# Kernel tuning notes

Hardware: AMD Instinct MI355X
Metric: run time of the kernel (lower is better)

## Reference

```python
import jax, jax.numpy as jnp
import numpy as np

N_NODES = 50000
N_EDGES = 800000
IN_DIM = 128
HGC = 128
LG = 3
K = 3
N_CLASSES = 10
BN_EPS = 1e-5


def setup_inputs() -> dict:
    key = jax.random.key(0)
    ks = jax.random.split(key, 16)
    inp = {
        "features": jax.random.normal(ks[0], (N_NODES, IN_DIM), dtype=jnp.float32),
        "edge_index": jax.random.randint(ks[1], (2, N_EDGES), 0, N_NODES, dtype=jnp.int64),
        "edge_weight": jax.random.uniform(ks[2], (N_EDGES,), dtype=jnp.float32),
    }
    # ChebConv weights: one (K, in, out) stack per layer (PyG: K separate bias-free Linears)
    dims = [IN_DIM] + [HGC] * LG
    for i in range(LG):
        fan_in = dims[i]
        inp[f"W{i}"] = jax.random.normal(ks[3 + i], (K, dims[i], dims[i + 1]), dtype=jnp.float32) * np.sqrt(2.0 / fan_in)
    # classifier head: Linear(HGC,256) -> ReLU -> BatchNorm1d(256) -> Linear(256, num_classes)
    inp["Wc1"] = jax.random.normal(ks[8], (HGC, 256), dtype=jnp.float32) * np.sqrt(2.0 / HGC)
    inp["bc1"] = jnp.zeros((256,), dtype=jnp.float32)
    inp["gamma"] = jnp.ones((256,), dtype=jnp.float32)
    inp["beta"] = jnp.zeros((256,), dtype=jnp.float32)
    inp["Wc2"] = jax.random.normal(ks[9], (256, N_CLASSES), dtype=jnp.float32) * np.sqrt(2.0 / 256)
    inp["bc2"] = jnp.zeros((N_CLASSES,), dtype=jnp.float32)
    return inp


def _scaled_laplacian_weights(edge_index, edge_weight, n_nodes):
    # get_laplacian(sym): L = I - D^{-1/2} A D^{-1/2}; ChebConv scales 2L/lambda_max - I
    # with lambda_max = 2.0 -> L_hat off-diagonal weights = -A_norm, diagonal = 0.
    row, col = edge_index[0], edge_index[1]
    deg = jax.ops.segment_sum(edge_weight, row, num_segments=n_nodes)
    dinv = jnp.where(deg > 0, jax.lax.rsqrt(jnp.maximum(deg, 1e-30)), 0.0)
    return -dinv[row] * edge_weight * dinv[col]


def _propagate(x, row, col, w, n_nodes):
    # SpMM: (L_hat @ x)[i] = sum_e w[e] * x[col[e]] for row[e]==i
    return jax.ops.segment_sum(w[:, None] * x[col], row, num_segments=n_nodes)


def _cheb_conv(x, W, row, col, w, n_nodes):
    # W: (K, in, out). Chebyshev recursion T0=x, T1=Lx, Tk=2LT_{k-1}-T_{k-2}
    Tx0 = x
    out = Tx0 @ W[0]
    Tx1 = _propagate(Tx0, row, col, w, n_nodes)
    out = out + Tx1 @ W[1]
    for k in range(2, W.shape[0]):
        Tx2 = 2.0 * _propagate(Tx1, row, col, w, n_nodes) - Tx0
        out = out + Tx2 @ W[k]
        Tx0, Tx1 = Tx1, Tx2
    return out


def reference(features, edge_index, edge_weight, W0, W1, W2, Wc1, bc1, gamma, beta, Wc2, bc2):
    n = features.shape[0]
    row, col = edge_index[0], edge_index[1]
    w = _scaled_laplacian_weights(edge_index, edge_weight, n)
    x = features
    for W in (W0, W1, W2):
        x = jax.nn.relu(_cheb_conv(x, W, row, col, w, n))  # dropout is identity in eval
    h = jax.nn.relu(x @ Wc1 + bc1)
    mean = jnp.mean(h, axis=0)
    var = jnp.var(h, axis=0)  # biased, as torch BatchNorm1d normalization
    h = (h - mean) * jax.lax.rsqrt(var + BN_EPS) * gamma + beta
    logit = h @ Wc2 + bc2
    return (logit, edge_weight)
```

## Files before the change

kernel.cpp:

```cpp
#include <hip/hip_runtime.h>
#include <cstdint>
#include <cstddef>

#define DIM 128
#define BN_EPS 1e-5f
#define NS 8

typedef short bf16x8 __attribute__((ext_vector_type(8)));
typedef float f32x4 __attribute__((ext_vector_type(4)));

__device__ __forceinline__ unsigned short f2bf(float f) {
  unsigned u = __float_as_uint(f);
  u = (u + 0x7fffu + ((u >> 16) & 1u)) >> 16;
  return (unsigned short)u;
}
__device__ __forceinline__ float bf2f(unsigned v) {
  return __uint_as_float(v << 16);
}


__global__ void deg_hist_kernel(const int* __restrict__ ei, const float* __restrict__ ew,
                                float* __restrict__ degS, int* __restrict__ countS, int E,
                                int N) {
  int e = blockIdx.x * blockDim.x + threadIdx.x;
  int g = blockIdx.x & (NS - 1);
  if (e < E) {
    int r = ei[e];
    atomicAdd(&degS[(size_t)g * N + r], ew[e]);
    atomicAdd(&countS[(size_t)g * N + r], 1);
  }
}

__global__ void reduce_dinv_kernel(const float* __restrict__ degS, float* __restrict__ dinv,
                                   int N) {
  int i = blockIdx.x * blockDim.x + threadIdx.x;
  if (i < N) {
    float d = 0.f;
#pragma unroll
    for (int g = 0; g < NS; ++g) d += degS[(size_t)g * N + i];
    dinv[i] = d > 0.f ? rsqrtf(fmaxf(d, 1e-30f)) : 0.f;
  }
}

__global__ __launch_bounds__(512) void scan_a_kernel(const int* __restrict__ countS,
                                                     int* __restrict__ off2,
                                                     int* __restrict__ bsums, int n8, int N) {
  __shared__ int sd[512];
  int t = threadIdx.x;
  int i = blockIdx.x * 512 + t;
  int v = 0;
  if (i < n8) {
    int g = i & (NS - 1), r = i >> 3;
    v = countS[(size_t)g * N + r];
  }
  sd[t] = v;
  __syncthreads();
  for (int off = 1; off < 512; off <<= 1) {
    int x = (t >= off) ? sd[t - off] : 0;
    __syncthreads();
    sd[t] += x;
    __syncthreads();
  }
  if (i < n8) off2[i] = sd[t] - v;
  if (t == 511) bsums[blockIdx.x] = sd[511];
}

__global__ __launch_bounds__(1024) void scan_b_kernel(int* __restrict__ bsums, int nb) {
  __shared__ int sd[1024];
  int t = threadIdx.x;
  int v = (t < nb) ? bsums[t] : 0;
  sd[t] = v;
  __syncthreads();
  for (int off = 1; off < 1024; off <<= 1) {
    int x = (t >= off) ? sd[t - off] : 0;
    __syncthreads();
    sd[t] += x;
    __syncthreads();
  }
  if (t < nb) bsums[t] = sd[t] - v;
}

__global__ __launch_bounds__(512) void scan_c_kernel(int* __restrict__ off2,
                                                     const int* __restrict__ bsums, int n8) {
  int i = blockIdx.x * 512 + threadIdx.x;
  if (i < n8) off2[i] += bsums[blockIdx.x];
}

__global__ void rowptr_kernel(const int* __restrict__ off2, int* __restrict__ row_ptr, int N,
                              int E) {
  int i = blockIdx.x * blockDim.x + threadIdx.x;
  if (i < N) row_ptr[i] = off2[i * NS];
  if (i == 0) row_ptr[N] = E;
}

__global__ void scatter_kernel(const int* __restrict__ ei, const float* __restrict__ ew,
                               const float* __restrict__ dinv, const int* __restrict__ off2,
                               int* __restrict__ cursorS, int2* __restrict__ cw, int E, int N) {
  int e = blockIdx.x * blockDim.x + threadIdx.x;
  int g = blockIdx.x & (NS - 1);
  if (e < E) {
    int r = ei[e], c = ei[E + e];
    float w = -dinv[r] * ew[e] * dinv[c];
    int pos = off2[r * NS + g] + atomicAdd(&cursorS[(size_t)g * N + r], 1);
    cw[pos] = make_int2(c, __float_as_int(w));
  }
}


__global__ void combine_weightsT_kernel(const float* __restrict__ W,
                                        unsigned short* __restrict__ WcatT) {
  int idx = blockIdx.x * blockDim.x + threadIdx.x;
  if (idx < DIM * DIM) {
    int i = idx >> 7, o = idx & 127;
    float w0 = W[i * DIM + o];
    float w1 = W[DIM * DIM + i * DIM + o];
    float w2 = W[2 * DIM * DIM + i * DIM + o];
    WcatT[(size_t)o * 384 + i] = f2bf(w0 - w2);
    WcatT[(size_t)o * 384 + 128 + i] = f2bf(w1);
    WcatT[(size_t)o * 384 + 256 + i] = f2bf(2.0f * w2);
  }
}

__global__ void wc1t_kernel(const float* __restrict__ Wc1, unsigned short* __restrict__ Wc1T) {
  int idx = blockIdx.x * blockDim.x + threadIdx.x;
  if (idx < 128 * 256) {
    int k = idx >> 8, n = idx & 255;
    Wc1T[(size_t)n * 128 + k] = f2bf(Wc1[(size_t)k * 256 + n]);
  }
}

__global__ void f2bf_kernel(const float* __restrict__ in, unsigned short* __restrict__ outp,
                            int n4) {
  int i = blockIdx.x * blockDim.x + threadIdx.x;
  if (i < n4) {
    float4 v = reinterpret_cast<const float4*>(in)[i];
    ushort4 o;
    o.x = f2bf(v.x); o.y = f2bf(v.y); o.z = f2bf(v.z); o.w = f2bf(v.w);
    reinterpret_cast<ushort4*>(outp)[i] = o;
  }
}


__global__ __launch_bounds__(256) void spmm_kernel(const int* __restrict__ row_ptr,
                                                   const int2* __restrict__ cw,
                                                   const unsigned short* __restrict__ X,
                                                   unsigned short* __restrict__ Y, int N) {
  int row = (blockIdx.x * blockDim.x + threadIdx.x) >> 6;
  int lane = threadIdx.x & 63;
  if (row >= N) return;
  int s = row_ptr[row], e = row_ptr[row + 1];
  float lo0 = 0.f, lo1 = 0.f, lo2 = 0.f, lo3 = 0.f, lo4 = 0.f, lo5 = 0.f, lo6 = 0.f, lo7 = 0.f;
  float hi0 = 0.f, hi1 = 0.f, hi2 = 0.f, hi3 = 0.f, hi4 = 0.f, hi5 = 0.f, hi6 = 0.f, hi7 = 0.f;
  int j = s;
  int lo2b = lane * 2;
  for (; j + 7 < e; j += 8) {
    int2 e0 = cw[j], e1 = cw[j + 1], e2 = cw[j + 2], e3 = cw[j + 3];
    int2 e4 = cw[j + 4], e5 = cw[j + 5], e6 = cw[j + 6], e7 = cw[j + 7];
    unsigned v0 = *reinterpret_cast<const unsigned*>(X + (size_t)e0.x * DIM + lo2b);
    unsigned v1 = *reinterpret_cast<const unsigned*>(X + (size_t)e1.x * DIM + lo2b);
    unsigned v2 = *reinterpret_cast<const unsigned*>(X + (size_t)e2.x * DIM + lo2b);
    unsigned v3 = *reinterpret_cast<const unsigned*>(X + (size_t)e3.x * DIM + lo2b);
    unsigned v4 = *reinterpret_cast<const unsigned*>(X + (size_t)e4.x * DIM + lo2b);
    unsigned v5 = *reinterpret_cast<const unsigned*>(X + (size_t)e5.x * DIM + lo2b);
    unsigned v6 = *reinterpret_cast<const unsigned*>(X + (size_t)e6.x * DIM + lo2b);
    unsigned v7 = *reinterpret_cast<const unsigned*>(X + (size_t)e7.x * DIM + lo2b);
    float w0 = __int_as_float(e0.y), w1 = __int_as_float(e1.y);
    float w2 = __int_as_float(e2.y), w3 = __int_as_float(e3.y);
    float w4 = __int_as_float(e4.y), w5 = __int_as_float(e5.y);
    float w6 = __int_as_float(e6.y), w7 = __int_as_float(e7.y);
    lo0 += w0 * bf2f(v0 & 0xffffu); hi0 += w0 * bf2f(v0 >> 16);
    lo1 += w1 * bf2f(v1 & 0xffffu); hi1 += w1 * bf2f(v1 >> 16);
    lo2 += w2 * bf2f(v2 & 0xffffu); hi2 += w2 * bf2f(v2 >> 16);
    lo3 += w3 * bf2f(v3 & 0xffffu); hi3 += w3 * bf2f(v3 >> 16);
    lo4 += w4 * bf2f(v4 & 0xffffu); hi4 += w4 * bf2f(v4 >> 16);
    lo5 += w5 * bf2f(v5 & 0xffffu); hi5 += w5 * bf2f(v5 >> 16);
    lo6 += w6 * bf2f(v6 & 0xffffu); hi6 += w6 * bf2f(v6 >> 16);
    lo7 += w7 * bf2f(v7 & 0xffffu); hi7 += w7 * bf2f(v7 >> 16);
  }
  for (; j + 1 < e; j += 2) {
    int2 e0 = cw[j], e1 = cw[j + 1];
    unsigned v0 = *reinterpret_cast<const unsigned*>(X + (size_t)e0.x * DIM + lo2b);
    unsigned v1 = *reinterpret_cast<const unsigned*>(X + (size_t)e1.x * DIM + lo2b);
    float w0 = __int_as_float(e0.y), w1 = __int_as_float(e1.y);
    lo0 += w0 * bf2f(v0 & 0xffffu); hi0 += w0 * bf2f(v0 >> 16);
    lo1 += w1 * bf2f(v1 & 0xffffu); hi1 += w1 * bf2f(v1 >> 16);
  }
  if (j < e) {
    int2 e0 = cw[j];
    unsigned v0 = *reinterpret_cast<const unsigned*>(X + (size_t)e0.x * DIM + lo2b);
    float w0 = __int_as_float(e0.y);
    lo0 += w0 * bf2f(v0 & 0xffffu);
    hi0 += w0 * bf2f(v0 >> 16);
  }
  float a0 = ((lo0 + lo1) + (lo2 + lo3)) + ((lo4 + lo5) + (lo6 + lo7));
  float a1 = ((hi0 + hi1) + (hi2 + hi3)) + ((hi4 + hi5) + (hi6 + hi7));
  unsigned o = (unsigned)f2bf(a0) | ((unsigned)f2bf(a1) << 16);
  *reinterpret_cast<unsigned*>(Y + (size_t)row * DIM + lo2b) = o;
}


__global__ __launch_bounds__(256) void gemm3_mfma_kernel(const unsigned short* __restrict__ X,
                                                         const unsigned short* __restrict__ S1,
                                                         const unsigned short* __restrict__ S2,
                                                         const unsigned short* __restrict__ BT,
                                                         unsigned short* __restrict__ out, int M) {
  __shared__ short As[128 * 40];
  __shared__ short Bs[128 * 40];
  int tid = threadIdx.x;
  int wv = tid >> 6, ln = tid & 63;
  int lg = ln >> 4, lr = ln & 15;
  int blockRow = blockIdx.x * 128;
  f32x4 acc[2][8];
#pragma unroll
  for (int m = 0; m < 2; ++m)
#pragma unroll
    for (int n = 0; n < 8; ++n) acc[m][n] = (f32x4){0.f, 0.f, 0.f, 0.f};
  const unsigned short* srcs[3] = {X, S1, S2};
  int srow = tid >> 1;
  int scol = (tid & 1) * 16;
  int arow = blockRow + srow;
  bool aok = arow < M;
  for (int seg = 0; seg < 3; ++seg) {
    const unsigned short* src = srcs[seg];
    for (int k0 = 0; k0 < DIM; k0 += 32) {
      float4 av0, av1;
      if (aok) {
        const float4* ap = reinterpret_cast<const float4*>(src + (size_t)arow * DIM + k0 + scol);
        av0 = ap[0];
        av1 = ap[1];
      } else {
        av0 = make_float4(0.f, 0.f, 0.f, 0.f);
        av1 = av0;
      }
      const float4* bp =
          reinterpret_cast<const float4*>(BT + (size_t)srow * 384 + seg * DIM + k0 + scol);
      float4 bv0 = bp[0], bv1 = bp[1];
      __syncthreads();
      *reinterpret_cast<float4*>(&As[srow * 40 + scol]) = av0;
      *reinterpret_cast<float4*>(&As[srow * 40 + scol + 8]) = av1;
      *reinterpret_cast<float4*>(&Bs[srow * 40 + scol]) = bv0;
      *reinterpret_cast<float4*>(&Bs[srow * 40 + scol + 8]) = bv1;
      __syncthreads();
      bf16x8 af[2], bf[8];
#pragma unroll
      for (int m = 0; m < 2; ++m)
        af[m] = *reinterpret_cast<const bf16x8*>(&As[(wv * 32 + m * 16 + lr) * 40 + lg * 8]);
#pragma unroll
      for (int n = 0; n < 8; ++n)
        bf[n] = *reinterpret_cast<const bf16x8*>(&Bs[(n * 16 + lr) * 40 + lg * 8]);
#pragma unroll
      for (int m = 0; m < 2; ++m)
#pragma unroll
        for (int n = 0; n < 8; ++n)
          acc[m][n] = __builtin_amdgcn_mfma_f32_16x16x32_bf16(af[m], bf[n], acc[m][n], 0, 0, 0);
    }
  }
#pragma unroll
  for (int m = 0; m < 2; ++m)
#pragma unroll
    for (int n = 0; n < 8; ++n) {
      int col = n * 16 + lr;
#pragma unroll
      for (int r = 0; r < 4; ++r) {
        int grow = blockRow + wv * 32 + m * 16 + lg * 4 + r;
        if (grow < M) out[(size_t)grow * DIM + col] = f2bf(fmaxf(acc[m][n][r], 0.f));
      }
    }
}


__global__ __launch_bounds__(256) void head_mfma_kernel(const unsigned short* __restrict__ X,
                                                        const unsigned short* __restrict__ BT,
                                                        const float* __restrict__ bc1,
                                                        unsigned short* __restrict__ h,
                                                        float* __restrict__ sums, int M) {
  __shared__ short As[128 * 40];
  __shared__ short Bs[128 * 40];
  int tid = threadIdx.x;
  int wv = tid >> 6, ln = tid & 63;
  int lg = ln >> 4, lr = ln & 15;
  int blockRow = blockIdx.x * 128;
  int n0 = blockIdx.y * 128;
  f32x4 acc[2][8];
#pragma unroll
  for (int m = 0; m < 2; ++m)
#pragma unroll
    for (int n = 0; n < 8; ++n) acc[m][n] = (f32x4){0.f, 0.f, 0.f, 0.f};
  int srow = tid >> 1;
  int scol = (tid & 1) * 16;
  int arow = blockRow + srow;
  bool aok = arow < M;
  for (int k0 = 0; k0 < DIM; k0 += 32) {
    float4 av0, av1;
    if (aok) {
      const float4* ap = reinterpret_cast<const float4*>(X + (size_t)arow * DIM + k0 + scol);
      av0 = ap[0];
      av1 = ap[1];
    } else {
      av0 = make_float4(0.f, 0.f, 0.f, 0.f);
      av1 = av0;
    }
    const float4* bp =
        reinterpret_cast<const float4*>(BT + (size_t)(n0 + srow) * DIM + k0 + scol);
    float4 bv0 = bp[0], bv1 = bp[1];
    __syncthreads();
    *reinterpret_cast<float4*>(&As[srow * 40 + scol]) = av0;
    *reinterpret_cast<float4*>(&As[srow * 40 + scol + 8]) = av1;
    *reinterpret_cast<float4*>(&Bs[srow * 40 + scol]) = bv0;
    *reinterpret_cast<float4*>(&Bs[srow * 40 + scol + 8]) = bv1;
    __syncthreads();
    bf16x8 af[2], bf[8];
#pragma unroll
    for (int m = 0; m < 2; ++m)
      af[m] = *reinterpret_cast<const bf16x8*>(&As[(wv * 32 + m * 16 + lr) * 40 + lg * 8]);
#pragma unroll
    for (int n = 0; n < 8; ++n)
      bf[n] = *reinterpret_cast<const bf16x8*>(&Bs[(n * 16 + lr) * 40 + lg * 8]);
#pragma unroll
    for (int m = 0; m < 2; ++m)
#pragma unroll
      for (int n = 0; n < 8; ++n)
        acc[m][n] = __builtin_amdgcn_mfma_f32_16x16x32_bf16(af[m], bf[n], acc[m][n], 0, 0, 0);
  }
  float psum[8], psq[8];
#pragma unroll
  for (int n = 0; n < 8; ++n) { psum[n] = 0.f; psq[n] = 0.f; }
#pragma unroll
  for (int m = 0; m < 2; ++m)
#pragma unroll
    for (int n = 0; n < 8; ++n) {
      int colg = n0 + n * 16 + lr;
      float bias = bc1[colg];
#pragma unroll
      for (int r = 0; r < 4; ++r) {
        int grow = blockRow + wv * 32 + m * 16 + lg * 4 + r;
        if (grow < M) {
          float v = fmaxf(acc[m][n][r] + bias, 0.f);
          h[(size_t)grow * 256 + colg] = f2bf(v);
          psum[n] += v;
          psq[n] += v * v;
        }
      }
    }
  float* Rs = reinterpret_cast<float*>(As);
  int rid = wv * 4 + lg;
  __syncthreads();
#pragma unroll
  for (int n = 0; n < 8; ++n) Rs[rid * 128 + n * 16 + lr] = psum[n];
  __syncthreads();
  if (tid < 128) {
    float s = 0.f;
#pragma unroll
    for (int r = 0; r < 16; ++r) s += Rs[r * 128 + tid];
    atomicAdd(&sums[n0 + tid], s);
  }
  __syncthreads();
#pragma unroll
  for (int n = 0; n < 8; ++n) Rs[rid * 128 + n * 16 + lr] = psq[n];
  __syncthreads();
  if (tid < 128) {
    float s = 0.f;
#pragma unroll
    for (int r = 0; r < 16; ++r) s += Rs[r * 128 + tid];
    atomicAdd(&sums[256 + n0 + tid], s);
  }
}

__global__ __launch_bounds__(256) void bnfold_kernel(const float* __restrict__ sums,
                                                     const float* __restrict__ gamma,
                                                     const float* __restrict__ beta,
                                                     const float* __restrict__ Wc2,
                                                     const float* __restrict__ bc2,
                                                     float* __restrict__ W2e,
                                                     float* __restrict__ b2e, int M) {
  __shared__ float bsh[256];
  int c = threadIdx.x;
  float mean = sums[c] / (float)M;
  float var = sums[256 + c] / (float)M - mean * mean;
  float a = gamma[c] * rsqrtf(var + BN_EPS);
  float b = beta[c] - mean * a;
  for (int j = 0; j < 10; ++j) W2e[c * 10 + j] = a * Wc2[c * 10 + j];
  bsh[c] = b;
  __syncthreads();
  if (c < 10) {
    float t = bc2[c];
    for (int k = 0; k < 256; ++k) t += bsh[k] * Wc2[k * 10 + c];
    b2e[c] = t;
  }
}


__global__ __launch_bounds__(256) void final_kernel(const unsigned short* __restrict__ h,
                                                    const float* __restrict__ W2e,
                                                    const float* __restrict__ b2e,
                                                    float* __restrict__ out, int M) {
  __shared__ float Ws[2560];
  __shared__ float bs[10];
  for (int i = threadIdx.x; i < 2560; i += 256) Ws[i] = W2e[i];
  if (threadIdx.x < 10) bs[threadIdx.x] = b2e[threadIdx.x];
  __syncthreads();
  int row = (blockIdx.x * blockDim.x + threadIdx.x) >> 6;
  int lane = threadIdx.x & 63;
  if (row >= M) return;
  uint2 hv = *reinterpret_cast<const uint2*>(h + (size_t)row * 256 + lane * 4);
  float hvv[4] = {bf2f(hv.x & 0xffffu), bf2f(hv.x >> 16), bf2f(hv.y & 0xffffu), bf2f(hv.y >> 16)};
  float p[10];
#pragma unroll
  for (int j = 0; j < 10; ++j) p[j] = 0.f;
#pragma unroll
  for (int t = 0; t < 4; ++t) {
    const float* wrow = &Ws[(lane * 4 + t) * 10];
#pragma unroll
    for (int j = 0; j < 10; ++j) p[j] += hvv[t] * wrow[j];
  }
#pragma unroll
  for (int off = 32; off > 0; off >>= 1)
#pragma unroll
    for (int j = 0; j < 10; ++j) p[j] += __shfl_down(p[j], off);
  if (lane == 0) {
#pragma unroll
    for (int j = 0; j < 10; ++j) out[(size_t)row * 10 + j] = p[j] + bs[j];
  }
}

__global__ void copy4_kernel(const float* __restrict__ src, float* __restrict__ dst, int n) {
  int i = blockIdx.x * blockDim.x + threadIdx.x;
  int i4 = i * 4;
  if (i4 + 3 < n) {
    reinterpret_cast<float4*>(dst)[i] = reinterpret_cast<const float4*>(src)[i];
  } else {
    for (int k = i4; k < n; ++k) dst[k] = src[k];
  }
}


extern "C" void kernel_launch(void* const* d_in, const int* in_sizes, int n_in,
                              void* d_out, int out_size, void* d_ws, size_t ws_size,
                              hipStream_t stream) {
  const float* features = (const float*)d_in[0];
  const int* ei = (const int*)d_in[1];
  const float* ew = (const float*)d_in[2];
  const float* W0 = (const float*)d_in[3];
  const float* W1 = (const float*)d_in[4];
  const float* W2 = (const float*)d_in[5];
  const float* Wc1 = (const float*)d_in[6];
  const float* bc1 = (const float*)d_in[7];
  const float* gamma = (const float*)d_in[8];
  const float* beta = (const float*)d_in[9];
  const float* Wc2 = (const float*)d_in[10];
  const float* bc2 = (const float*)d_in[11];
  float* out = (float*)d_out;

  const int N = in_sizes[0] / DIM;
  const int E = in_sizes[2];
  const int n8 = N * NS;

  size_t off = 0;
  auto alloc = [&](size_t bytes) -> void* {
    void* p = (char*)d_ws + off;
    off += (bytes + 511) & ~(size_t)511;
    return p;
  };
  float* dinv = (float*)alloc((size_t)N * 4);
  float* degS = (float*)alloc((size_t)n8 * 4);
  int* countS = (int*)alloc((size_t)n8 * 4);
  int* cursorS = (int*)alloc((size_t)n8 * 4);
  int* off2 = (int*)alloc((size_t)(n8 + NS) * 4);
  int* bsums = (int*)alloc(1024 * 4);
  int* row_ptr = (int*)alloc((size_t)(N + 1) * 4);
  int2* cw = (int2*)alloc((size_t)E * 8);
  unsigned short* featbf = (unsigned short*)alloc((size_t)N * DIM * 2);
  unsigned short* xbuf = (unsigned short*)alloc((size_t)N * DIM * 2);
  unsigned short* S1 = (unsigned short*)alloc((size_t)N * DIM * 2);
  unsigned short* S2 = (unsigned short*)alloc((size_t)N * DIM * 2);
  unsigned short* h = (unsigned short*)alloc((size_t)N * 256 * 2);
  unsigned short* WcatT = (unsigned short*)alloc((size_t)3 * 128 * 384 * 2);
  unsigned short* Wc1T = (unsigned short*)alloc((size_t)256 * 128 * 2);
  float* W2e = (float*)alloc(2560 * 4);
  float* b2e = (float*)alloc(16 * 4);
  float* sums = (float*)alloc(512 * 4);

  hipMemsetAsync(degS, 0, (size_t)n8 * 4, stream);
  hipMemsetAsync(countS, 0, (size_t)n8 * 4, stream);
  hipMemsetAsync(cursorS, 0, (size_t)n8 * 4, stream);
  hipMemsetAsync(sums, 0, 512 * 4, stream);

  int eb = (E + 255) / 256;
  int nb = (N + 255) / 256;
  int sa_blocks = (n8 + 511) / 512;

  f2bf_kernel<<<(N * DIM / 4 + 255) / 256, 256, 0, stream>>>(features, featbf, N * DIM / 4);
  deg_hist_kernel<<<eb, 256, 0, stream>>>(ei, ew, degS, countS, E, N);
  reduce_dinv_kernel<<<nb, 256, 0, stream>>>(degS, dinv, N);
  scan_a_kernel<<<sa_blocks, 512, 0, stream>>>(countS, off2, bsums, n8, N);
  scan_b_kernel<<<1, 1024, 0, stream>>>(bsums, sa_blocks);
  scan_c_kernel<<<sa_blocks, 512, 0, stream>>>(off2, bsums, n8);
  rowptr_kernel<<<nb, 256, 0, stream>>>(off2, row_ptr, N, E);
  scatter_kernel<<<eb, 256, 0, stream>>>(ei, ew, dinv, off2, cursorS, cw, E, N);

  for (int l = 0; l < 3; ++l) {
    const float* Wl = (l == 0) ? W0 : (l == 1) ? W1 : W2;
    combine_weightsT_kernel<<<(DIM * DIM + 255) / 256, 256, 0, stream>>>(
        Wl, WcatT + (size_t)l * 128 * 384);
  }
  wc1t_kernel<<<(128 * 256 + 255) / 256, 256, 0, stream>>>(Wc1, Wc1T);

  int spmm_blocks = (N + 3) / 4;
  int gemm_blocks = (N + 127) / 128;
  for (int l = 0; l < 3; ++l) {
    const unsigned short* X = (l == 0) ? featbf : xbuf;
    spmm_kernel<<<spmm_blocks, 256, 0, stream>>>(row_ptr, cw, X, S1, N);
    spmm_kernel<<<spmm_blocks, 256, 0, stream>>>(row_ptr, cw, S1, S2, N);
    gemm3_mfma_kernel<<<gemm_blocks, 256, 0, stream>>>(X, S1, S2, WcatT + (size_t)l * 128 * 384,
                                                       xbuf, N);
  }

  dim3 hgrid(gemm_blocks, 2);
  head_mfma_kernel<<<hgrid, 256, 0, stream>>>(xbuf, Wc1T, bc1, h, sums, N);
  bnfold_kernel<<<1, 256, 0, stream>>>(sums, gamma, beta, Wc2, bc2, W2e, b2e, N);
  final_kernel<<<(N + 3) / 4, 256, 0, stream>>>(h, W2e, b2e, out, N);
  copy4_kernel<<<(E / 4 + 255) / 256, 256, 0, stream>>>(ew, out + (size_t)N * 10, E);
}
```

Measured before the change: 498.1 us.

## Pack degree and count into one 64-bit atomic and merge preprocessing launches

The degree histogram now accumulates fixed-point edge weight and edge count in one 64-bit atomic per edge. The returned old count is stored as the edge's slot, so the scatter kernel no longer needs a second atomic cursor pass. The row_ptr kernel is folded into the scan finalisation, the three weight-combine launches become one 2D launch, and three memsets become one. Edge weights are now quantised to 2^-24 fixed point before the degree sum, which adds rounding error and risks overflow for nodes with very large weighted degree.

```diff
diff --git a/kernel.cpp b/kernel.cpp
--- a/kernel.cpp
+++ b/kernel.cpp
@@ -5,6 +5,7 @@
 #define DIM 128
 #define BN_EPS 1e-5f
 #define NS 8
+#define FIX_SCALE 16777216.0f
 
 typedef short bf16x8 __attribute__((ext_vector_type(8)));
 typedef float f32x4 __attribute__((ext_vector_type(4)));
@@ -20,29 +21,33 @@
 
 
 __global__ void deg_hist_kernel(const int* __restrict__ ei, const float* __restrict__ ew,
-                                float* __restrict__ degS, int* __restrict__ countS, int E,
-                                int N) {
+                                unsigned long long* __restrict__ pck,
+                                unsigned* __restrict__ eidx, int E, int N) {
   int e = blockIdx.x * blockDim.x + threadIdx.x;
   int g = blockIdx.x & (NS - 1);
   if (e < E) {
     int r = ei[e];
-    atomicAdd(&degS[(size_t)g * N + r], ew[e]);
-    atomicAdd(&countS[(size_t)g * N + r], 1);
-  }
-}
-
-__global__ void reduce_dinv_kernel(const float* __restrict__ degS, float* __restrict__ dinv,
-                                   int N) {
+    unsigned fix = (unsigned)(ew[e] * FIX_SCALE + 0.5f);
+    unsigned long long old =
+        atomicAdd(&pck[(size_t)g * N + r], (1ull << 32) | (unsigned long long)fix);
+    eidx[e] = (unsigned)(old >> 32);
+  }
+}
+
+__global__ void reduce_dinv_kernel(const unsigned long long* __restrict__ pck,
+                                   float* __restrict__ dinv, int N) {
   int i = blockIdx.x * blockDim.x + threadIdx.x;
   if (i < N) {
     float d = 0.f;
 #pragma unroll
-    for (int g = 0; g < NS; ++g) d += degS[(size_t)g * N + i];
+    for (int g = 0; g < NS; ++g)
+      d += (float)(unsigned)(pck[(size_t)g * N + i] & 0xffffffffull);
+    d *= (1.0f / FIX_SCALE);
     dinv[i] = d > 0.f ? rsqrtf(fmaxf(d, 1e-30f)) : 0.f;
   }
 }
 
-__global__ __launch_bounds__(512) void scan_a_kernel(const int* __restrict__ countS,
+__global__ __launch_bounds__(512) void scan_a_kernel(const unsigned long long* __restrict__ pck,
                                                      int* __restrict__ off2,
                                                      int* __restrict__ bsums, int n8, int N) {
   __shared__ int sd[512];
@@ -51,7 +56,7 @@
   int v = 0;
   if (i < n8) {
     int g = i & (NS - 1), r = i >> 3;
-    v = countS[(size_t)g * N + r];
+    v = (int)(pck[(size_t)g * N + r] >> 32);
   }
   sd[t] = v;
   __syncthreads();
@@ -81,43 +86,49 @@
 }
 
 __global__ __launch_bounds__(512) void scan_c_kernel(int* __restrict__ off2,
-                                                     const int* __restrict__ bsums, int n8) {
+                                                     const int* __restrict__ bsums,
+                                                     int* __restrict__ row_ptr, int n8, int N,
+                                                     int E) {
   int i = blockIdx.x * 512 + threadIdx.x;
-  if (i < n8) off2[i] += bsums[blockIdx.x];
-}
-
-__global__ void rowptr_kernel(const int* __restrict__ off2, int* __restrict__ row_ptr, int N,
-                              int E) {
-  int i = blockIdx.x * blockDim.x + threadIdx.x;
-  if (i < N) row_ptr[i] = off2[i * NS];
-  if (i == 0) row_ptr[N] = E;
+  if (i < n8) {
+    int v = off2[i] + bsums[blockIdx.x];
+    off2[i] = v;
+    if ((i & (NS - 1)) == 0) row_ptr[i >> 3] = v;
+  }
+  if (blockIdx.x == 0 && threadIdx.x == 0) row_ptr[N] = E;
 }
 
 __global__ void scatter_kernel(const int* __restrict__ ei, const float* __restrict__ ew,
                                const float* __restrict__ dinv, const int* __restrict__ off2,
-                               int* __restrict__ cursorS, int2* __restrict__ cw, int E, int N) {
+                               const unsigned* __restrict__ eidx, int2* __restrict__ cw, int E,
+                               int N) {
   int e = blockIdx.x * blockDim.x + threadIdx.x;
   int g = blockIdx.x & (NS - 1);
   if (e < E) {
     int r = ei[e], c = ei[E + e];
     float w = -dinv[r] * ew[e] * dinv[c];
-    int pos = off2[r * NS + g] + atomicAdd(&cursorS[(size_t)g * N + r], 1);
+    int pos = off2[r * NS + g] + (int)eidx[e];
     cw[pos] = make_int2(c, __float_as_int(w));
   }
 }
 
 
-__global__ void combine_weightsT_kernel(const float* __restrict__ W,
+__global__ void combine_weightsT_kernel(const float* __restrict__ W0,
+                                        const float* __restrict__ W1,
+                                        const float* __restrict__ W2,
                                         unsigned short* __restrict__ WcatT) {
+  int l = blockIdx.y;
+  const float* W = (l == 0) ? W0 : (l == 1) ? W1 : W2;
+  unsigned short* outp = WcatT + (size_t)l * 128 * 384;
   int idx = blockIdx.x * blockDim.x + threadIdx.x;
   if (idx < DIM * DIM) {
     int i = idx >> 7, o = idx & 127;
     float w0 = W[i * DIM + o];
     float w1 = W[DIM * DIM + i * DIM + o];
     float w2 = W[2 * DIM * DIM + i * DIM + o];
-    WcatT[(size_t)o * 384 + i] = f2bf(w0 - w2);
-    WcatT[(size_t)o * 384 + 128 + i] = f2bf(w1);
-    WcatT[(size_t)o * 384 + 256 + i] = f2bf(2.0f * w2);
+    outp[(size_t)o * 384 + i] = f2bf(w0 - w2);
+    outp[(size_t)o * 384 + 128 + i] = f2bf(w1);
+    outp[(size_t)o * 384 + 256 + i] = f2bf(2.0f * w2);
   }
 }
 
@@ -462,9 +473,8 @@
     return p;
   };
   float* dinv = (float*)alloc((size_t)N * 4);
-  float* degS = (float*)alloc((size_t)n8 * 4);
-  int* countS = (int*)alloc((size_t)n8 * 4);
-  int* cursorS = (int*)alloc((size_t)n8 * 4);
+  unsigned long long* pck = (unsigned long long*)alloc((size_t)n8 * 8);
+  unsigned* eidx = (unsigned*)alloc((size_t)E * 4);
   int* off2 = (int*)alloc((size_t)(n8 + NS) * 4);
   int* bsums = (int*)alloc(1024 * 4);
   int* row_ptr = (int*)alloc((size_t)(N + 1) * 4);
@@ -480,9 +490,7 @@
   float* b2e = (float*)alloc(16 * 4);
   float* sums = (float*)alloc(512 * 4);
 
-  hipMemsetAsync(degS, 0, (size_t)n8 * 4, stream);
-  hipMemsetAsync(countS, 0, (size_t)n8 * 4, stream);
-  hipMemsetAsync(cursorS, 0, (size_t)n8 * 4, stream);
+  hipMemsetAsync(pck, 0, (size_t)n8 * 8, stream);
   hipMemsetAsync(sums, 0, 512 * 4, stream);
 
   int eb = (E + 255) / 256;
@@ -490,19 +498,15 @@
   int sa_blocks = (n8 + 511) / 512;
 
   f2bf_kernel<<<(N * DIM / 4 + 255) / 256, 256, 0, stream>>>(features, featbf, N * DIM / 4);
-  deg_hist_kernel<<<eb, 256, 0, stream>>>(ei, ew, degS, countS, E, N);
-  reduce_dinv_kernel<<<nb, 256, 0, stream>>>(degS, dinv, N);
-  scan_a_kernel<<<sa_blocks, 512, 0, stream>>>(countS, off2, bsums, n8, N);
+  deg_hist_kernel<<<eb, 256, 0, stream>>>(ei, ew, pck, eidx, E, N);
+  reduce_dinv_kernel<<<nb, 256, 0, stream>>>(pck, dinv, N);
+  scan_a_kernel<<<sa_blocks, 512, 0, stream>>>(pck, off2, bsums, n8, N);
   scan_b_kernel<<<1, 1024, 0, stream>>>(bsums, sa_blocks);
-  scan_c_kernel<<<sa_blocks, 512, 0, stream>>>(off2, bsums, n8);
-  rowptr_kernel<<<nb, 256, 0, stream>>>(off2, row_ptr, N, E);
-  scatter_kernel<<<eb, 256, 0, stream>>>(ei, ew, dinv, off2, cursorS, cw, E, N);
-
-  for (int l = 0; l < 3; ++l) {
-    const float* Wl = (l == 0) ? W0 : (l == 1) ? W1 : W2;
-    combine_weightsT_kernel<<<(DIM * DIM + 255) / 256, 256, 0, stream>>>(
-        Wl, WcatT + (size_t)l * 128 * 384);
-  }
+  scan_c_kernel<<<sa_blocks, 512, 0, stream>>>(off2, bsums, row_ptr, n8, N, E);
+  scatter_kernel<<<eb, 256, 0, stream>>>(ei, ew, dinv, off2, eidx, cw, E, N);
+
+  dim3 cwgrid((DIM * DIM + 255) / 256, 3);
+  combine_weightsT_kernel<<<cwgrid, 256, 0, stream>>>(W0, W1, W2, WcatT);
   wc1t_kernel<<<(128 * 256 + 255) / 256, 256, 0, stream>>>(Wc1, Wc1T);
 
   int spmm_blocks = (N + 3) / 4;
```

After: 437.4 us. 1.14x faster.
